# Performance work log

Hardware: AMD Instinct MI355X
Metric: run time of the kernel (lower is better)

## Reference

```python
import jax, jax.numpy as jnp
import numpy as np

B, L, D, H = 2, 2048, 1024, 16
HD = D // H  # head_dim = 64


def setup_inputs() -> dict:
    key = jax.random.key(0)
    k1, k2, k3 = jax.random.split(key, 3)
    x = jax.random.normal(k1, (B, L, D), dtype=jnp.float32)
    # nn.Linear(d_model, 3*d_model): weight [3D, D], bias [3D]
    lim = 1.0 / np.sqrt(D)
    W_qkv = jax.random.uniform(k2, (3 * D, D), dtype=jnp.float32, minval=-lim, maxval=lim)
    b_qkv = jax.random.uniform(k3, (3 * D,), dtype=jnp.float32, minval=-lim, maxval=lim)
    return {"x": x, "W_qkv": W_qkv, "b_qkv": b_qkv}


def reference(x, W_qkv, b_qkv):
    b, l, d = x.shape
    qkv = x @ W_qkv.T + b_qkv                      # [b, l, 3d]
    q, k, v = jnp.split(qkv, 3, axis=-1)           # each [b, l, d]
    # split heads: [b, l, h, hd]
    q = q.reshape(b, l, H, HD)
    k = k.reshape(b, l, H, HD)
    v = v.reshape(b, l, H, HD)
    scale = 1.0 / np.sqrt(HD).astype(np.float32)
    # scores [b, h, l, l]
    scores = jnp.einsum('bqhd,bkhd->bhqk', q, k) * scale
    attn = jax.nn.softmax(scores, axis=-1)
    out = jnp.einsum('bhqk,bkhd->bqhd', attn, v)   # [b, l, h, hd]
    return out.reshape(b, l, d)
```

## Files before the change

kernel.cpp:

```cpp
#include <hip/hip_runtime.h>

#define BATCH 2
#define SEQ 2048
#define DMODEL 1024
#define NH 16
#define HD 64
#define M_TOT (BATCH*SEQ)
#define N_TOT (3*DMODEL)
#define K_TOT (DMODEL)
#define NQK   (2*DMODEL)
#define QSCALE 0.18033688011112042f

typedef __attribute__((ext_vector_type(8)))  _Float16 f16x8;
typedef __attribute__((ext_vector_type(4)))  float    f32x4;
typedef __attribute__((ext_vector_type(16))) float    f32x16;

static __device__ __forceinline__ unsigned short f2h(float f) {
  _Float16 h = (_Float16)f;
  return __builtin_bit_cast(unsigned short, h);
}

static __device__ __forceinline__ f32x16 zero16() {
  f32x16 z;
  #pragma unroll
  for (int i = 0; i < 16; ++i) z[i] = 0.f;
  return z;
}

static __device__ __forceinline__ void async16(const unsigned short* g, unsigned short* l) {
  __builtin_amdgcn_global_load_lds(
      (const __attribute__((address_space(1))) unsigned*)g,
      (__attribute__((address_space(3))) unsigned*)l, 16, 0, 0);
}

static __device__ __forceinline__ void barrier_fenced() {
  asm volatile("" ::: "memory");
  __builtin_amdgcn_sched_barrier(0);
  __builtin_amdgcn_s_barrier();
  __builtin_amdgcn_sched_barrier(0);
  asm volatile("" ::: "memory");
}

__global__ __launch_bounds__(256) void cast_f16_2(
    const float* __restrict__ xsrc, const float* __restrict__ wsrc,
    unsigned short* __restrict__ xdst, unsigned short* __restrict__ wdst,
    int n8x, int n8tot)
{
  int i = blockIdx.x * 256 + threadIdx.x;
  if (i >= n8tot) return;
  const float* src;
  unsigned short* dst;
  int idx;
  if (i < n8x) { src = xsrc; dst = xdst; idx = i; }
  else         { src = wsrc; dst = wdst; idx = i - n8x; }
  float4 v0 = ((const float4*)src)[2*idx];
  float4 v1 = ((const float4*)src)[2*idx + 1];
  uint4 pk;
  pk.x = (unsigned)f2h(v0.x) | ((unsigned)f2h(v0.y) << 16);
  pk.y = (unsigned)f2h(v0.z) | ((unsigned)f2h(v0.w) << 16);
  pk.z = (unsigned)f2h(v1.x) | ((unsigned)f2h(v1.y) << 16);
  pk.w = (unsigned)f2h(v1.z) | ((unsigned)f2h(v1.w) << 16);
  ((uint4*)dst)[idx] = pk;
}

__global__ __launch_bounds__(256) void qkv_gemm_mfma(
    const unsigned short* __restrict__ Xh,
    const unsigned short* __restrict__ Wh,
    const float* __restrict__ bias,
    unsigned short* __restrict__ QK,
    unsigned short* __restrict__ VT)
{
  __shared__ unsigned short As[3][128][32];
  __shared__ unsigned short Bs[3][128][32];

  const int tid  = threadIdx.x;
  const int wave = tid >> 6;
  const int lane = tid & 63;
  const int l15  = lane & 15;
  const int quad = lane >> 4;

  const bool isV = (blockIdx.x >= (NQK/128));
  const int n0 = (isV ? (blockIdx.x - NQK/128) : blockIdx.x) * 128;
  const int m0 = blockIdx.y * 128;

  const unsigned short* Arows = isV ? (Wh + (size_t)(NQK + n0) * K_TOT)
                                    : (Xh + (size_t)m0 * K_TOT);
  const unsigned short* Brows = isV ? (Xh + (size_t)m0 * K_TOT)
                                    : (Wh + (size_t)n0 * K_TOT);

  const int srow = tid >> 2;
  const int skc  = (tid & 3) * 8;
  const unsigned short* Ag0 = Arows + (size_t)srow * K_TOT + skc;
  const unsigned short* Ag1 = Arows + (size_t)(64 + srow) * K_TOT + skc;
  const unsigned short* Bg0 = Brows + (size_t)srow * K_TOT + skc;
  const unsigned short* Bg1 = Brows + (size_t)(64 + srow) * K_TOT + skc;
  unsigned short* Al = &As[0][0][0] + tid * 8;
  unsigned short* Bl = &Bs[0][0][0] + tid * 8;

  const int wm = (wave & 1) * 64;
  const int wn = (wave >> 1) * 64;

  f32x4 acc[4][4];
  #pragma unroll
  for (int i = 0; i < 4; ++i)
    #pragma unroll
    for (int j = 0; j < 4; ++j) acc[i][j] = (f32x4){0.f,0.f,0.f,0.f};

  auto STAGE = [&](int k0, int bb) {
    async16(Ag0 + k0, Al + bb*4096);
    async16(Ag1 + k0, Al + bb*4096 + 2048);
    async16(Bg0 + k0, Bl + bb*4096);
    async16(Bg1 + k0, Bl + bb*4096 + 2048);
  };

  auto COMPUTE = [&](int bb) {
    f16x8 af[4], bf[4];
    #pragma unroll
    for (int i = 0; i < 4; ++i)
      af[i] = *(const f16x8*)&As[bb][wm + i*16 + l15][quad*8];
    #pragma unroll
    for (int j = 0; j < 4; ++j)
      bf[j] = *(const f16x8*)&Bs[bb][wn + j*16 + l15][quad*8];
    #pragma unroll
    for (int i = 0; i < 4; ++i)
      #pragma unroll
      for (int j = 0; j < 4; ++j)
        acc[i][j] = __builtin_amdgcn_mfma_f32_16x16x32_f16(af[i], bf[j], acc[i][j], 0, 0, 0);
  };

  STAGE(0, 0);
  STAGE(32, 1);
  int bs = 2, bc = 0;
  for (int t = 0; t < K_TOT/32 - 2; ++t) {
    asm volatile("s_waitcnt vmcnt(4)" ::: "memory");
    barrier_fenced();
    STAGE((t+2)*32, bs);
    COMPUTE(bc);
    bs = (bs == 2) ? 0 : bs + 1;
    bc = (bc == 2) ? 0 : bc + 1;
  }
  asm volatile("s_waitcnt vmcnt(4)" ::: "memory");
  barrier_fenced();
  COMPUTE(bc);
  bc = (bc == 2) ? 0 : bc + 1;
  asm volatile("s_waitcnt vmcnt(0)" ::: "memory");
  barrier_fenced();
  COMPUTE(bc);

  if (!isV) {
    const float sc = (n0 < DMODEL) ? QSCALE : 1.0f;
    float bv[4];
    #pragma unroll
    for (int j = 0; j < 4; ++j) bv[j] = bias[n0 + wn + j*16 + l15];
    #pragma unroll
    for (int i = 0; i < 4; ++i)
      #pragma unroll
      for (int j = 0; j < 4; ++j)
        #pragma unroll
        for (int r = 0; r < 4; ++r) {
          const size_t row = (size_t)(m0 + wm + i*16 + quad*4 + r);
          QK[row * NQK + n0 + wn + j*16 + l15] = f2h((acc[i][j][r] + bv[j]) * sc);
        }
  } else {
    const int bidx  = m0 >> 11;
    const int sbase = (m0 & 2047) + wn;
    #pragma unroll
    for (int i = 0; i < 4; ++i)
      #pragma unroll
      for (int r = 0; r < 4; ++r) {
        const int nn = n0 + wm + i*16 + quad*4 + r;
        const float bb = bias[NQK + nn];
        unsigned short* drow =
            VT + ((size_t)(bidx*NH + (nn >> 6)) * HD + (nn & 63)) * SEQ + sbase;
        #pragma unroll
        for (int j = 0; j < 4; ++j)
          drow[j*16 + l15] = f2h(acc[i][j][r] + bb);
      }
  }
}

__global__ __launch_bounds__(256) void attn_mfma3(
    const unsigned short* __restrict__ QK,
    const unsigned short* __restrict__ VT,
    float* __restrict__ out)
{
  __shared__ unsigned short Ks[3][64][64];
  __shared__ unsigned short Vs[3][64][64];
  __shared__ unsigned short Ps[4][32][72];
  __shared__ float Dn[4][32];

  const int tid  = threadIdx.x;
  const int wv   = tid >> 6;
  const int lane = tid & 63;
  const int l31  = lane & 31;
  const int h32  = lane >> 5;
  const int qsw  = l31 >> 3;

  const int qt = blockIdx.x;
  const int hh = blockIdx.y;
  const int b  = blockIdx.z;
  const int q0 = qt*128 + wv*32;

  f16x8 qf[4];
  {
    const unsigned short* qrow = QK + (size_t)(b*SEQ + q0 + l31) * NQK + hh*HD;
    #pragma unroll
    for (int f = 0; f < 4; ++f)
      qf[f] = *(const f16x8*)(qrow + f*16 + h32*8);
  }

  const unsigned short* Kg = QK + (size_t)b*SEQ*NQK + DMODEL + hh*HD;
  const unsigned short* Vg = VT + (size_t)(b*NH + hh) * HD * SEQ;

  const int sr = tid >> 3;
  const int sp = tid & 7;
  const int sg = ((sp - sr) & 7) * 8;

  const unsigned short* kg0 = Kg + (size_t)sr      * NQK + sg;
  const unsigned short* kg1 = Kg + (size_t)(sr+32) * NQK + sg;
  const unsigned short* vg0 = Vg + (size_t)sr      * SEQ + sg;
  const unsigned short* vg1 = Vg + (size_t)(sr+32) * SEQ + sg;
  unsigned short* kl = &Ks[0][0][0] + tid*8;
  unsigned short* vl = &Vs[0][0][0] + tid*8;

  f32x16 oacc[2];
  oacc[0] = zero16();
  oacc[1] = zero16();
  float dsum = 0.f;

  auto STAGE = [&](int kt, int bb) {
    const size_t krow = (size_t)kt * 64 * NQK;
    const int    kcol = kt * 64;
    async16(kg0 + krow, kl + bb*4096);
    async16(kg1 + krow, kl + bb*4096 + 2048);
    async16(vg0 + kcol, vl + bb*4096);
    async16(vg1 + kcol, vl + bb*4096 + 2048);
  };

  auto COMPUTE = [&](int bb) {
    const unsigned short* ks = &Ks[bb][0][0];
    const unsigned short* vs = &Vs[bb][0][0];

    f32x16 sa[2];
    sa[0] = zero16();
    sa[1] = zero16();
    __builtin_amdgcn_s_setprio(1);
    #pragma unroll
    for (int f = 0; f < 4; ++f) {
      const int g = f*2 + h32;
      #pragma unroll
      for (int kb = 0; kb < 2; ++kb) {
        const int row = kb*32 + l31;
        f16x8 kf = *(const f16x8*)(ks + row*64 + ((g + row) & 7) * 8);
        sa[kb] = __builtin_amdgcn_mfma_f32_32x32x16_f16(kf, qf[f], sa[kb], 0, 0, 0);
      }
    }
    __builtin_amdgcn_s_setprio(0);

    #pragma unroll
    for (int kb = 0; kb < 2; ++kb) {
      #pragma unroll
      for (int g4 = 0; g4 < 4; ++g4) {
        unsigned short hsv[4];
        #pragma unroll
        for (int r = 0; r < 4; ++r) {
          float p = exp2f(sa[kb][g4*4 + r]);
          dsum += p;
          hsv[r] = f2h(p);
        }
        unsigned short* dst =
            &Ps[wv][l31][(((kb*4 + g4) ^ qsw) & 7) * 8 + h32*4];
        uint2 pk;
        pk.x = (unsigned)hsv[0] | ((unsigned)hsv[1] << 16);
        pk.y = (unsigned)hsv[2] | ((unsigned)hsv[3] << 16);
        *(uint2*)dst = pk;
      }
    }

    __builtin_amdgcn_s_setprio(1);
    #pragma unroll
    for (int f = 0; f < 4; ++f) {
      const int g = f*2 + h32;
      f16x8 pf = *(const f16x8*)&Ps[wv][l31][((g ^ qsw) & 7) * 8];
      #pragma unroll
      for (int jd = 0; jd < 2; ++jd) {
        const int row = jd*32 + l31;
        f16x8 vf = *(const f16x8*)(vs + row*64 + ((g + row) & 7) * 8);
        oacc[jd] = __builtin_amdgcn_mfma_f32_32x32x16_f16(pf, vf, oacc[jd], 0, 0, 0);
      }
    }
    __builtin_amdgcn_s_setprio(0);
  };

  STAGE(0, 0);
  STAGE(1, 1);
  int bs = 2, bc = 0;
  for (int kt = 0; kt < SEQ/64 - 2; ++kt) {
    asm volatile("s_waitcnt vmcnt(4)" ::: "memory");
    barrier_fenced();
    STAGE(kt + 2, bs);
    COMPUTE(bc);
    bs = (bs == 2) ? 0 : bs + 1;
    bc = (bc == 2) ? 0 : bc + 1;
  }
  asm volatile("s_waitcnt vmcnt(4)" ::: "memory");
  barrier_fenced();
  COMPUTE(bc);
  bc = (bc == 2) ? 0 : bc + 1;
  asm volatile("s_waitcnt vmcnt(0)" ::: "memory");
  barrier_fenced();
  COMPUTE(bc);

  dsum += __shfl_xor(dsum, 32, 64);
  Dn[wv][l31] = 1.f / dsum;

  #pragma unroll
  for (int jd = 0; jd < 2; ++jd) {
    #pragma unroll
    for (int g4 = 0; g4 < 4; ++g4) {
      #pragma unroll
      for (int r = 0; r < 4; ++r) {
        const int qrow = g4*8 + h32*4 + r;
        const float oval = oacc[jd][g4*4 + r] * Dn[wv][qrow];
        out[(size_t)(b*SEQ + q0 + qrow) * DMODEL + hh*HD + jd*32 + l31] = oval;
      }
    }
  }
}

extern "C" void kernel_launch(void* const* d_in, const int* in_sizes, int n_in,
                              void* d_out, int out_size, void* d_ws, size_t ws_size,
                              hipStream_t stream) {
  const float* x    = (const float*)d_in[0];
  const float* W    = (const float*)d_in[1];
  const float* bias = (const float*)d_in[2];
  float* out = (float*)d_out;

  unsigned short* qk = (unsigned short*)d_ws;
  unsigned short* vt = qk + (size_t)M_TOT * NQK;
  unsigned short* xh = vt + (size_t)BATCH * NH * HD * SEQ;
  unsigned short* wh = xh + (size_t)M_TOT * K_TOT;

  const int n8x = M_TOT*K_TOT/8;
  const int n8w = N_TOT*K_TOT/8;
  cast_f16_2<<<(n8x + n8w + 255)/256, 256, 0, stream>>>(x, W, xh, wh, n8x, n8x + n8w);

  dim3 g1(N_TOT/128, M_TOT/128);
  qkv_gemm_mfma<<<g1, 256, 0, stream>>>(xh, wh, bias, qk, vt);

  dim3 g2(SEQ/128, NH, BATCH);
  attn_mfma3<<<g2, 256, 0, stream>>>(qk, vt, out);
}
```

Before: 187.6 us.

## Remap block order, unroll pipelines, switch attention to double buffering

The QKV GEMM and attention kernels remap block indices so that neighbouring blocks spread across XCDs or chiplets for better L2 locality. The GEMM K-loop is unrolled by three with constant buffer indices. The attention kernel moves from a triple-buffered to a double-buffered K/V pipeline with an extra barrier per step, which frees LDS and may raise occupancy. It also drops the sched_barriers around s_barrier and splits the softmax denominator into four partial sums to shorten the dependency chain. The trade-off is less prefetch depth in attention and possibly looser instruction scheduling around barriers.

```diff
diff --git a/kernel.cpp b/kernel.cpp
--- a/kernel.cpp
+++ b/kernel.cpp
@@ -33,11 +33,9 @@
       (__attribute__((address_space(3))) unsigned*)l, 16, 0, 0);
 }
 
-static __device__ __forceinline__ void barrier_fenced() {
+static __device__ __forceinline__ void barrier_f() {
   asm volatile("" ::: "memory");
-  __builtin_amdgcn_sched_barrier(0);
   __builtin_amdgcn_s_barrier();
-  __builtin_amdgcn_sched_barrier(0);
   asm volatile("" ::: "memory");
 }
 
@@ -79,9 +77,15 @@
   const int l15  = lane & 15;
   const int quad = lane >> 4;
 
-  const bool isV = (blockIdx.x >= (NQK/128));
-  const int n0 = (isV ? (blockIdx.x - NQK/128) : blockIdx.x) * 128;
-  const int m0 = blockIdx.y * 128;
+  const int lin = blockIdx.x + blockIdx.y * 24;
+  const int c   = lin & 7;
+  const int w   = lin >> 3;
+  const int bxl = (c & 1) * 12 + (w % 12);
+  const int byl = (c >> 1) * 8 + (w / 12);
+
+  const bool isV = (bxl >= (NQK/128));
+  const int n0 = (isV ? (bxl - NQK/128) : bxl) * 128;
+  const int m0 = byl * 128;
 
   const unsigned short* Arows = isV ? (Wh + (size_t)(NQK + n0) * K_TOT)
                                     : (Xh + (size_t)m0 * K_TOT);
@@ -128,24 +132,26 @@
         acc[i][j] = __builtin_amdgcn_mfma_f32_16x16x32_f16(af[i], bf[j], acc[i][j], 0, 0, 0);
   };
 
+  #define G_KSTEP(t, sb, cb) \
+    asm volatile("s_waitcnt vmcnt(4)" ::: "memory"); \
+    barrier_f(); \
+    STAGE(((t)+2)*32, (sb)); \
+    COMPUTE((cb));
+
   STAGE(0, 0);
   STAGE(32, 1);
-  int bs = 2, bc = 0;
-  for (int t = 0; t < K_TOT/32 - 2; ++t) {
-    asm volatile("s_waitcnt vmcnt(4)" ::: "memory");
-    barrier_fenced();
-    STAGE((t+2)*32, bs);
-    COMPUTE(bc);
-    bs = (bs == 2) ? 0 : bs + 1;
-    bc = (bc == 2) ? 0 : bc + 1;
+  for (int t = 0; t < 30; t += 3) {
+    G_KSTEP(t,   2, 0)
+    G_KSTEP(t+1, 0, 1)
+    G_KSTEP(t+2, 1, 2)
   }
   asm volatile("s_waitcnt vmcnt(4)" ::: "memory");
-  barrier_fenced();
-  COMPUTE(bc);
-  bc = (bc == 2) ? 0 : bc + 1;
+  barrier_f();
+  COMPUTE(0);
   asm volatile("s_waitcnt vmcnt(0)" ::: "memory");
-  barrier_fenced();
-  COMPUTE(bc);
+  barrier_f();
+  COMPUTE(1);
+  #undef G_KSTEP
 
   if (!isV) {
     const float sc = (n0 < DMODEL) ? QSCALE : 1.0f;
@@ -184,8 +190,8 @@
     const unsigned short* __restrict__ VT,
     float* __restrict__ out)
 {
-  __shared__ unsigned short Ks[3][64][64];
-  __shared__ unsigned short Vs[3][64][64];
+  __shared__ unsigned short Ks[2][64][64];
+  __shared__ unsigned short Vs[2][64][64];
   __shared__ unsigned short Ps[4][32][72];
   __shared__ float Dn[4][32];
 
@@ -196,9 +202,12 @@
   const int h32  = lane >> 5;
   const int qsw  = l31 >> 3;
 
-  const int qt = blockIdx.x;
-  const int hh = blockIdx.y;
-  const int b  = blockIdx.z;
+  const int lin = blockIdx.x + ((blockIdx.y + (blockIdx.z << 4)) << 4);
+  const int logical = ((lin & 7) << 6) + (lin >> 3);
+  const int qt   = logical & 15;
+  const int head = logical >> 4;
+  const int hh   = head & 15;
+  const int b    = head >> 4;
   const int q0 = qt*128 + wv*32;
 
   f16x8 qf[4];
@@ -226,7 +235,7 @@
   f32x16 oacc[2];
   oacc[0] = zero16();
   oacc[1] = zero16();
-  float dsum = 0.f;
+  float dsv[4] = {0.f, 0.f, 0.f, 0.f};
 
   auto STAGE = [&](int kt, int bb) {
     const size_t krow = (size_t)kt * 64 * NQK;
@@ -265,7 +274,7 @@
         #pragma unroll
         for (int r = 0; r < 4; ++r) {
           float p = exp2f(sa[kb][g4*4 + r]);
-          dsum += p;
+          dsv[r] += p;
           hsv[r] = f2h(p);
         }
         unsigned short* dst =
@@ -292,25 +301,25 @@
     __builtin_amdgcn_s_setprio(0);
   };
 
+  #define A_STEP(kt, sb, cb) \
+    STAGE((kt)+1, (sb)); \
+    asm volatile("s_waitcnt vmcnt(4)" ::: "memory"); \
+    barrier_f(); \
+    COMPUTE((cb)); \
+    barrier_f();
+
   STAGE(0, 0);
-  STAGE(1, 1);
-  int bs = 2, bc = 0;
-  for (int kt = 0; kt < SEQ/64 - 2; ++kt) {
-    asm volatile("s_waitcnt vmcnt(4)" ::: "memory");
-    barrier_fenced();
-    STAGE(kt + 2, bs);
-    COMPUTE(bc);
-    bs = (bs == 2) ? 0 : bs + 1;
-    bc = (bc == 2) ? 0 : bc + 1;
-  }
-  asm volatile("s_waitcnt vmcnt(4)" ::: "memory");
-  barrier_fenced();
-  COMPUTE(bc);
-  bc = (bc == 2) ? 0 : bc + 1;
+  for (int kt = 0; kt < 30; kt += 2) {
+    A_STEP(kt,   1, 0)
+    A_STEP(kt+1, 0, 1)
+  }
+  A_STEP(30, 1, 0)
   asm volatile("s_waitcnt vmcnt(0)" ::: "memory");
-  barrier_fenced();
-  COMPUTE(bc);
-
+  barrier_f();
+  COMPUTE(1);
+  #undef A_STEP
+
+  float dsum = (dsv[0] + dsv[1]) + (dsv[2] + dsv[3]);
   dsum += __shfl_xor(dsum, 32, 64);
   Dn[wv][l31] = 1.f / dsum;
 
```

Measured after the change: 183.2 us. 2.4% less time.
